# Performance work log

Hardware: AMD Instinct MI355X
Metric: run time of the kernel (lower is better)

The kernel has to match this reference:

```python
import jax, jax.numpy as jnp
import numpy as np

TAU = 2.0      # LIF membrane time constant
ALPHA = 4.0    # spikingjelly surrogate.Sigmoid default alpha
V_TH = 1.0     # LIF threshold
EPS = 1e-5     # BatchNorm eps
NUM_HEADS = 8
TOPK = 64      # int(0.25 * 256)


@jax.custom_vjp
def spike_fn(x):
    # Heaviside spike with sigmoid surrogate gradient
    return (x >= 0.0).astype(x.dtype)

def _spike_fwd(x):
    return spike_fn(x), x

def _spike_bwd(x, g):
    s = jax.nn.sigmoid(ALPHA * x)
    return (g * ALPHA * s * (1.0 - s),)

spike_fn.defvjp(_spike_fwd, _spike_bwd)


def lif(x_seq):
    # Multi-step LIF (decay_input=True, hard reset to 0, detach_reset=True).
    # x_seq: [T, ...]; returns spikes of same shape.
    def step(v, x):
        v = v + (x - v) / TAU
        s = spike_fn(v - V_TH)
        v = v * (1.0 - jax.lax.stop_gradient(s))
        return v, s
    _, spikes = jax.lax.scan(step, jnp.zeros_like(x_seq[0]), x_seq)
    return spikes


def bn_eval(x, p):
    # BatchNorm in eval mode over last axis; p rows = [gamma, beta, mean, var]
    gamma, beta, mean, var = p[0], p[1], p[2], p[3]
    return (x - mean) * (gamma * jax.lax.rsqrt(var + EPS)) + beta


def setup_inputs() -> dict:
    key = jax.random.key(0)
    ks = jax.random.split(key, 10)
    T, B, N, C, H = 4, 16, 256, 256, NUM_HEADS
    w_scale = C ** -0.5
    return {
        "x": jax.random.normal(ks[0], (T, B, N, C), jnp.float32),
        "wq": jax.random.normal(ks[1], (C, C), jnp.float32) * w_scale,
        "wk": jax.random.normal(ks[2], (C, C), jnp.float32) * w_scale,
        "wv": jax.random.normal(ks[3], (C, C), jnp.float32) * w_scale,
        "bnq": jax.random.uniform(ks[4], (4, C), jnp.float32, 0.1, 1.0),
        "bnk": jax.random.uniform(ks[5], (4, C), jnp.float32, 0.1, 1.0),
        "bnv": jax.random.uniform(ks[6], (4, C), jnp.float32, 0.1, 1.0),
        "proj_w": jax.random.normal(ks[7], (C, C), jnp.float32) * w_scale,
        "proj_bn": jax.random.uniform(ks[8], (4, C), jnp.float32, 0.1, 1.0),
        "rel_bias_table": jax.random.normal(ks[9], (2 * N - 1, H), jnp.float32),
    }


def reference(x, wq, wk, wv, bnq, bnk, bnv, proj_w, proj_bn, rel_bias_table):
    T, B, N, C = x.shape
    H = NUM_HEADS
    D = C // H
    scale = C ** -0.5

    def qkv_branch(w, bn_p):
        h = jnp.einsum('tbnc,oc->tbno', x, w)   # Linear (no bias)
        h = bn_eval(h, bn_p)                    # eval BN is per-channel affine
        s = lif(h)                              # [T,B,N,C] spikes
        return s.reshape(T, B, N, H, D).transpose(0, 1, 3, 2, 4)  # [T,B,H,N,D]

    q = qkv_branch(wq, bnq)
    k = qkv_branch(wk, bnk)
    v = qkv_branch(wv, bnv)

    attn = jnp.einsum('tbhnd,tbhmd->tbhnm', q, k) * scale  # [T,B,H,N,N]

    # relative position bias gather: table[(j - i) + (N-1)] -> [N,N,H]
    rel_idx = (jnp.arange(N)[None, :] - jnp.arange(N)[:, None]) + (N - 1)
    rel_bias = rel_bias_table[rel_idx]                      # [N,N,H]
    attn = attn + rel_bias.transpose(2, 0, 1)[None, None]   # bcast over T,B

    # top-k keep per row, others zeroed (no softmax)
    kth = jax.lax.stop_gradient(jax.lax.top_k(attn, TOPK)[0][..., -1:])
    attn = jnp.where(attn >= kth, attn, 0.0)

    out = jnp.einsum('tbhnm,tbhmd->tbhnd', attn, v)
    out = out.transpose(0, 1, 3, 2, 4).reshape(T, B, N, C)
    out = lif(out)  # attn_lif

    # proj SpikLinearLayer: Linear -> BN(eval) -> LIF
    h = jnp.einsum('tbnc,oc->tbno', out, proj_w)
    h = bn_eval(h, proj_bn)
    return lif(h)
```

## Files before the change

### kernel.cpp

```cpp
#include <hip/hip_runtime.h>

typedef unsigned int u32;
typedef unsigned long long u64;

#define T_ 4
#define B_ 16
#define N_ 256
#define C_ 256
#define H_ 8
#define D_ 32
#define BNC_ 1048576
#define NELEM 4194304

__global__ __launch_bounds__(128) void gemm_bn(
    const float* __restrict__ A, const float* __restrict__ W,
    const float* __restrict__ bnp, float* __restrict__ Out)
{
  __shared__ float As[32][132];
  __shared__ float Ws[32][68];
  const int tid = threadIdx.x;
  const int m0 = blockIdx.y << 7;
  const int n0 = blockIdx.x << 6;
  const int tx = tid & 7;
  const int ty = tid >> 3;

  float acc[8][8] = {};
  float4 pa[8], pb[4];

#define LOADA(k0)                                                          \
  _Pragma("unroll") for (int c = 0; c < 8; ++c) {                          \
    int id2 = tid + (c << 7); int row = id2 >> 3; int k4 = (id2 & 7) << 2; \
    pa[c] = *(const float4*)(A + (size_t)(m0 + row) * 256 + (k0) + k4);    \
  }
#define LOADB(k0)                                                          \
  _Pragma("unroll") for (int c = 0; c < 4; ++c) {                          \
    int id2 = tid + (c << 7); int row = id2 >> 3; int k4 = (id2 & 7) << 2; \
    pb[c] = *(const float4*)(W + (size_t)(n0 + row) * 256 + (k0) + k4);    \
  }

  LOADA(0); LOADB(0);

  for (int s = 0; s < 8; ++s) {
#pragma unroll
    for (int c = 0; c < 8; ++c) {
      int id2 = tid + (c << 7); int row = id2 >> 3; int k4 = (id2 & 7) << 2;
      As[k4+0][row] = pa[c].x; As[k4+1][row] = pa[c].y;
      As[k4+2][row] = pa[c].z; As[k4+3][row] = pa[c].w;
    }
#pragma unroll
    for (int c = 0; c < 4; ++c) {
      int id2 = tid + (c << 7); int row = id2 >> 3; int k4 = (id2 & 7) << 2;
      Ws[k4+0][row] = pb[c].x; Ws[k4+1][row] = pb[c].y;
      Ws[k4+2][row] = pb[c].z; Ws[k4+3][row] = pb[c].w;
    }
    __syncthreads();
    if (s < 7) { int k0n = (s + 1) << 5; LOADA(k0n); LOADB(k0n); }
#pragma unroll
    for (int kk = 0; kk < 32; ++kk) {
      float4 a0 = *(const float4*)&As[kk][ty << 3];
      float4 a1 = *(const float4*)&As[kk][(ty << 3) + 4];
      float4 b0 = *(const float4*)&Ws[kk][tx << 3];
      float4 b1 = *(const float4*)&Ws[kk][(tx << 3) + 4];
      float av[8] = {a0.x,a0.y,a0.z,a0.w,a1.x,a1.y,a1.z,a1.w};
      float bv[8] = {b0.x,b0.y,b0.z,b0.w,b1.x,b1.y,b1.z,b1.w};
#pragma unroll
      for (int ii = 0; ii < 8; ++ii)
#pragma unroll
        for (int jj = 0; jj < 8; ++jj)
          acc[ii][jj] = fmaf(av[ii], bv[jj], acc[ii][jj]);
    }
    __syncthreads();
  }

  const float* gma = bnp;
  const float* bta = bnp + 256;
  const float* mea = bnp + 512;
  const float* vra = bnp + 768;
  float sc[8], me[8], be[8];
#pragma unroll
  for (int jj = 0; jj < 8; ++jj) {
    int o = n0 + (tx << 3) + jj;
    sc[jj] = __fmul_rn(gma[o], 1.0f / sqrtf(__fadd_rn(vra[o], 1e-5f)));
    me[jj] = mea[o];
    be[jj] = bta[o];
  }
#pragma unroll
  for (int ii = 0; ii < 8; ++ii) {
    int row = m0 + (ty << 3) + ii;
    float4 y0, y1;
    y0.x = __fadd_rn(__fmul_rn(__fsub_rn(acc[ii][0], me[0]), sc[0]), be[0]);
    y0.y = __fadd_rn(__fmul_rn(__fsub_rn(acc[ii][1], me[1]), sc[1]), be[1]);
    y0.z = __fadd_rn(__fmul_rn(__fsub_rn(acc[ii][2], me[2]), sc[2]), be[2]);
    y0.w = __fadd_rn(__fmul_rn(__fsub_rn(acc[ii][3], me[3]), sc[3]), be[3]);
    y1.x = __fadd_rn(__fmul_rn(__fsub_rn(acc[ii][4], me[4]), sc[4]), be[4]);
    y1.y = __fadd_rn(__fmul_rn(__fsub_rn(acc[ii][5], me[5]), sc[5]), be[5]);
    y1.z = __fadd_rn(__fmul_rn(__fsub_rn(acc[ii][6], me[6]), sc[6]), be[6]);
    y1.w = __fadd_rn(__fmul_rn(__fsub_rn(acc[ii][7], me[7]), sc[7]), be[7]);
    *(float4*)(Out + (size_t)row * 256 + n0 + (tx << 3))     = y0;
    *(float4*)(Out + (size_t)row * 256 + n0 + (tx << 3) + 4) = y1;
  }
}

__global__ __launch_bounds__(256) void lif_pack3(
    const float* __restrict__ h0, const float* __restrict__ h1,
    const float* __restrict__ h2,
    u32* __restrict__ m0p, u32* __restrict__ m1p, u32* __restrict__ m2p)
{
  const float* h = (blockIdx.y == 0) ? h0 : (blockIdx.y == 1) ? h1 : h2;
  u32* mask      = (blockIdx.y == 0) ? m0p : (blockIdx.y == 1) ? m1p : m2p;
  const int blk = blockIdx.x;
  const int b = blk >> 8, n = blk & 255;
  const int c = threadIdx.x;
  const int wave = c >> 6, lane = c & 63;
  const size_t idx = ((size_t)b * 256 + n) * 256 + c;
  float v = 0.0f;
#pragma unroll
  for (int t = 0; t < 4; ++t) {
    float xv = h[idx + (size_t)t * BNC_];
    v = __fadd_rn(v, __fmul_rn(__fsub_rn(xv, v), 0.5f));
    bool s = (v >= 1.0f);
    u64 bal = __ballot(s);
    const int h0i = wave << 1;
    u32* mptr = mask + ((size_t)(t * 16 + b) * 8) * 256 + n;
    if (lane == 0)  mptr[(size_t)h0i * 256]       = (u32)bal;
    if (lane == 32) mptr[(size_t)(h0i + 1) * 256] = (u32)(bal >> 32);
    v = s ? 0.0f : v;
  }
}

__global__ __launch_bounds__(256) void attn_topk_pv(
    const u32* __restrict__ qmask, const u32* __restrict__ kmask,
    const u32* __restrict__ vmask, const float* __restrict__ table,
    float* __restrict__ outPV)
{
  __shared__ __align__(16) float bias[511];
  __shared__ __align__(16) u64 comp[4][2][132];

  const int tbh = blockIdx.x;
  const int rg = blockIdx.y;
  const int hh = tbh & 7;
  const int tid = threadIdx.x;

  bias[tid] = table[tid * 8 + hh];
  if (tid < 255) bias[256 + tid] = table[(256 + tid) * 8 + hh];
  __syncthreads();

  const int wave = tid >> 6, lane = tid & 63;
  const int d = lane & 31, half = lane >> 5;

  u32 kmr[4], vmr[4];
#pragma unroll
  for (int r = 0; r < 4; ++r) {
    kmr[r] = kmask[((size_t)tbh << 8) + lane + (r << 6)];
    vmr[r] = vmask[((size_t)tbh << 8) + lane + (r << 6)];
  }
  const u64 below = (1ull << lane) - 1ull;
  u64* const clo = &comp[wave][0][0];
  u64* const chi = &comp[wave][1][0];

#pragma unroll 1
  for (int it = 0; it < 8; ++it) {
    const int i = (rg << 5) + (it << 2) + wave;
    const u32 qm = qmask[((size_t)tbh << 8) + i];
    float a[4]; u32 u[4];
#pragma unroll
    for (int r = 0; r < 4; ++r) {
      const int j = lane + (r << 6);
      const int m = __popc(qm & kmr[r]);
      float av = __fmul_rn((float)m, 0.0625f);
      av = __fadd_rn(av, bias[j - i + 255]);
      a[r] = av;
      const u32 bb = __float_as_uint(av);
      u[r] = bb ^ ((u32)((int)bb >> 31) | 0x80000000u);
    }
    u32 t = 0u;
    for (int bit = 31; bit >= 0; --bit) {
      const u32 cand = t | (1u << bit);
      const int cnt = __popcll(__ballot(u[0] >= cand)) +
                      __popcll(__ballot(u[1] >= cand)) +
                      __popcll(__ballot(u[2] >= cand)) +
                      __popcll(__ballot(u[3] >= cand));
      if (cnt >= 64) { t = cand; if (cnt == 64) break; }
    }
    const u64 B0 = __ballot(u[0] >= t), B1 = __ballot(u[1] >= t);
    const u64 B2 = __ballot(u[2] >= t), B3 = __ballot(u[3] >= t);
    const int c0 = __popcll(B0), c1 = __popcll(B1);
    const int c2 = __popcll(B2), c3 = __popcll(B3);
    const int p0 = __popcll(B0 & below);
    const int p1 = c0 + __popcll(B1 & below);
    const int p2 = __popcll(B2 & below);
    const int p3 = c2 + __popcll(B3 & below);
    if (u[0] >= t) clo[p0] = ((u64)vmr[0] << 32) | (u64)__float_as_uint(a[0]);
    if (u[1] >= t) clo[p1] = ((u64)vmr[1] << 32) | (u64)__float_as_uint(a[1]);
    if (u[2] >= t) chi[p2] = ((u64)vmr[2] << 32) | (u64)__float_as_uint(a[2]);
    if (u[3] >= t) chi[p3] = ((u64)vmr[3] << 32) | (u64)__float_as_uint(a[3]);
    const int nlo = c0 + c1, nhi = c2 + c3;
    if (lane < 2)      clo[nlo + lane] = 0ull;
    else if (lane < 4) chi[nhi + lane - 2] = 0ull;
    asm volatile("s_waitcnt lgkmcnt(0)" ::: "memory");

    const int n = half ? nhi : nlo;
    const u64* cp = half ? chi : clo;
    const int gn = (n + 1) >> 1;
    float s = 0.0f;
    for (int g = 0; g < gn; ++g) {
      uint4 e = *(const uint4*)(cp + ((size_t)g << 1));
      const u32 mk0 = (u32)__builtin_amdgcn_sbfe((int)e.y, d, 1);
      s = __fadd_rn(s, __uint_as_float(e.x & mk0));
      const u32 mk1 = (u32)__builtin_amdgcn_sbfe((int)e.w, d, 1);
      s = __fadd_rn(s, __uint_as_float(e.z & mk1));
    }
    s += __shfl_xor(s, 32, 64);
    if (half == 0)
      outPV[(((size_t)tbh << 8) + i) * 32 + d] = s;
  }
}

__global__ __launch_bounds__(256) void attn_lif(
    const float* __restrict__ pv, float* __restrict__ sout)
{
  const int blk = blockIdx.x;
  const int b = blk >> 8, n = blk & 255;
  const int c = threadIdx.x;
  const int hh = c >> 5, d = c & 31;
  float v = 0.0f;
#pragma unroll
  for (int t = 0; t < 4; ++t) {
    float xv = pv[(((size_t)(t * 16 + b) * 8 + hh) << 13) + (n << 5) + d];
    v = __fadd_rn(v, __fmul_rn(__fsub_rn(xv, v), 0.5f));
    bool s = (v >= 1.0f);
    sout[(((size_t)(t * 16 + b) << 8) + n) * 256 + c] = s ? 1.0f : 0.0f;
    v = s ? 0.0f : v;
  }
}

__global__ __launch_bounds__(256) void final_lif(
    const float* __restrict__ hp, float* __restrict__ out)
{
  const size_t base = (size_t)blockIdx.x * 256 + threadIdx.x;
  float v = 0.0f;
#pragma unroll
  for (int t = 0; t < 4; ++t) {
    float xv = hp[base + (size_t)t * BNC_];
    v = __fadd_rn(v, __fmul_rn(__fsub_rn(xv, v), 0.5f));
    bool s = (v >= 1.0f);
    out[base + (size_t)t * BNC_] = s ? 1.0f : 0.0f;
    v = s ? 0.0f : v;
  }
}

extern "C" void kernel_launch(void* const* d_in, const int* in_sizes, int n_in,
                              void* d_out, int out_size, void* d_ws, size_t ws_size,
                              hipStream_t stream) {
  const float* x       = (const float*)d_in[0];
  const float* wq      = (const float*)d_in[1];
  const float* wk      = (const float*)d_in[2];
  const float* wv      = (const float*)d_in[3];
  const float* bnq     = (const float*)d_in[4];
  const float* bnk     = (const float*)d_in[5];
  const float* bnv     = (const float*)d_in[6];
  const float* proj_w  = (const float*)d_in[7];
  const float* proj_bn = (const float*)d_in[8];
  const float* rtable  = (const float*)d_in[9];
  float* out = (float*)d_out;

  float* ws = (float*)d_ws;
  float* hq = ws;
  float* hk = ws + (size_t)NELEM;
  float* hv = ws + (size_t)NELEM * 2;
  u32* mq = (u32*)(ws + (size_t)NELEM * 3);
  u32* mk = mq + 131072;
  u32* mv = mk + 131072;
  float* outPV = hq;
  float* sout  = hk;
  float* hproj = hv;

  dim3 ggrid(4, 128);
  gemm_bn<<<ggrid, 128, 0, stream>>>(x, wq, bnq, hq);
  gemm_bn<<<ggrid, 128, 0, stream>>>(x, wk, bnk, hk);
  gemm_bn<<<ggrid, 128, 0, stream>>>(x, wv, bnv, hv);

  lif_pack3<<<dim3(4096, 3), 256, 0, stream>>>(hq, hk, hv, mq, mk, mv);

  attn_topk_pv<<<dim3(512, 8), 256, 0, stream>>>(mq, mk, mv, rtable, outPV);

  attn_lif<<<4096, 256, 0, stream>>>(outPV, sout);

  gemm_bn<<<ggrid, 128, 0, stream>>>(sout, proj_w, proj_bn, hproj);

  final_lif<<<4096, 256, 0, stream>>>(hproj, out);
}
```

Before: 335.3 us.

## Fuse QKV GEMMs into one kernel sharing A tile, with pre-transposed weights

Replaces the per-weight shared-memory tiled GEMM with a templated kernel that stages one 256-row A tile in LDS and reads the weights directly from global memory as a pre-transposed layout. Q, K and V are computed in a single launch that reuses the same A tile across all three weights. A new transpose kernel rewrites all four weight matrices each call. This cuts three launches and three reads of x down to one, but the weight operand now comes from cache/global instead of LDS with a 4xCW register tile per lane. Double-buffered prefetch is also dropped.

```diff
diff --git a/kernel.cpp b/kernel.cpp
--- a/kernel.cpp
+++ b/kernel.cpp
@@ -12,92 +12,110 @@
 #define BNC_ 1048576
 #define NELEM 4194304
 
-__global__ __launch_bounds__(128) void gemm_bn(
-    const float* __restrict__ A, const float* __restrict__ W,
-    const float* __restrict__ bnp, float* __restrict__ Out)
-{
-  __shared__ float As[32][132];
-  __shared__ float Ws[32][68];
+__global__ __launch_bounds__(256) void transpose4(
+    const float* __restrict__ w0, const float* __restrict__ w1,
+    const float* __restrict__ w2, const float* __restrict__ w3,
+    float* __restrict__ wt)
+{
+  __shared__ float t[32][33];
+  const float* src = (blockIdx.z == 0) ? w0 : (blockIdx.z == 1) ? w1
+                   : (blockIdx.z == 2) ? w2 : w3;
+  float* dst = wt + ((size_t)blockIdx.z << 16);
+  const int lx = threadIdx.x & 31, ly = threadIdx.x >> 5;
+  const int x = (blockIdx.x << 5) + lx;
+  const int y0 = (blockIdx.y << 5) + ly;
+#pragma unroll
+  for (int r = 0; r < 32; r += 8)
+    t[ly + r][lx] = src[(size_t)(y0 + r) * 256 + x];
+  __syncthreads();
+  const int xo = (blockIdx.y << 5) + lx;
+  const int yo = (blockIdx.x << 5) + ly;
+#pragma unroll
+  for (int r = 0; r < 32; r += 8)
+    dst[(size_t)(yo + r) * 256 + xo] = t[lx][ly + r];
+}
+
+template<int NW, int CW>
+__global__ __launch_bounds__(256) void gemm_bn_t(
+    const float* __restrict__ A, const float* __restrict__ WTb,
+    const float* __restrict__ bn0, const float* __restrict__ bn1,
+    const float* __restrict__ bn2,
+    float* __restrict__ O0, float* __restrict__ O1, float* __restrict__ O2)
+{
+  __shared__ float As[32][260];
   const int tid = threadIdx.x;
-  const int m0 = blockIdx.y << 7;
-  const int n0 = blockIdx.x << 6;
-  const int tx = tid & 7;
-  const int ty = tid >> 3;
-
-  float acc[8][8] = {};
-  float4 pa[8], pb[4];
-
-#define LOADA(k0)                                                          \
-  _Pragma("unroll") for (int c = 0; c < 8; ++c) {                          \
-    int id2 = tid + (c << 7); int row = id2 >> 3; int k4 = (id2 & 7) << 2; \
-    pa[c] = *(const float4*)(A + (size_t)(m0 + row) * 256 + (k0) + k4);    \
-  }
-#define LOADB(k0)                                                          \
-  _Pragma("unroll") for (int c = 0; c < 4; ++c) {                          \
-    int id2 = tid + (c << 7); int row = id2 >> 3; int k4 = (id2 & 7) << 2; \
-    pb[c] = *(const float4*)(W + (size_t)(n0 + row) * 256 + (k0) + k4);    \
-  }
-
-  LOADA(0); LOADB(0);
+  const int wave = tid >> 6, lane = tid & 63;
+  const int m0 = blockIdx.y << 8;
+  const int col0 = blockIdx.x * (4 * CW) + wave * CW;
+  const int sr = tid >> 3;
+  const int sk = (tid & 7) << 2;
+  const int row4 = lane << 2;
+
+  const float* bnp[3] = {bn0, bn1, bn2};
+  float* Op[3] = {O0, O1, O2};
+
+  float acc[NW][4][CW] = {};
 
   for (int s = 0; s < 8; ++s) {
+    const int k0 = s << 5;
+    float4 pa[8];
+#pragma unroll
+    for (int c = 0; c < 8; ++c)
+      pa[c] = *(const float4*)(A + (size_t)(m0 + sr + (c << 5)) * 256 + k0 + sk);
+    __syncthreads();
 #pragma unroll
     for (int c = 0; c < 8; ++c) {
-      int id2 = tid + (c << 7); int row = id2 >> 3; int k4 = (id2 & 7) << 2;
-      As[k4+0][row] = pa[c].x; As[k4+1][row] = pa[c].y;
-      As[k4+2][row] = pa[c].z; As[k4+3][row] = pa[c].w;
-    }
-#pragma unroll
-    for (int c = 0; c < 4; ++c) {
-      int id2 = tid + (c << 7); int row = id2 >> 3; int k4 = (id2 & 7) << 2;
-      Ws[k4+0][row] = pb[c].x; Ws[k4+1][row] = pb[c].y;
-      Ws[k4+2][row] = pb[c].z; Ws[k4+3][row] = pb[c].w;
+      As[sk + 0][sr + (c << 5)] = pa[c].x;
+      As[sk + 1][sr + (c << 5)] = pa[c].y;
+      As[sk + 2][sr + (c << 5)] = pa[c].z;
+      As[sk + 3][sr + (c << 5)] = pa[c].w;
     }
     __syncthreads();
-    if (s < 7) { int k0n = (s + 1) << 5; LOADA(k0n); LOADB(k0n); }
-#pragma unroll
+#pragma unroll 4
     for (int kk = 0; kk < 32; ++kk) {
-      float4 a0 = *(const float4*)&As[kk][ty << 3];
-      float4 a1 = *(const float4*)&As[kk][(ty << 3) + 4];
-      float4 b0 = *(const float4*)&Ws[kk][tx << 3];
-      float4 b1 = *(const float4*)&Ws[kk][(tx << 3) + 4];
-      float av[8] = {a0.x,a0.y,a0.z,a0.w,a1.x,a1.y,a1.z,a1.w};
-      float bv[8] = {b0.x,b0.y,b0.z,b0.w,b1.x,b1.y,b1.z,b1.w};
-#pragma unroll
-      for (int ii = 0; ii < 8; ++ii)
-#pragma unroll
-        for (int jj = 0; jj < 8; ++jj)
-          acc[ii][jj] = fmaf(av[ii], bv[jj], acc[ii][jj]);
-    }
-    __syncthreads();
-  }
-
-  const float* gma = bnp;
-  const float* bta = bnp + 256;
-  const float* mea = bnp + 512;
-  const float* vra = bnp + 768;
-  float sc[8], me[8], be[8];
-#pragma unroll
-  for (int jj = 0; jj < 8; ++jj) {
-    int o = n0 + (tx << 3) + jj;
-    sc[jj] = __fmul_rn(gma[o], 1.0f / sqrtf(__fadd_rn(vra[o], 1e-5f)));
-    me[jj] = mea[o];
-    be[jj] = bta[o];
-  }
-#pragma unroll
-  for (int ii = 0; ii < 8; ++ii) {
-    int row = m0 + (ty << 3) + ii;
-    float4 y0, y1;
-    y0.x = __fadd_rn(__fmul_rn(__fsub_rn(acc[ii][0], me[0]), sc[0]), be[0]);
-    y0.y = __fadd_rn(__fmul_rn(__fsub_rn(acc[ii][1], me[1]), sc[1]), be[1]);
-    y0.z = __fadd_rn(__fmul_rn(__fsub_rn(acc[ii][2], me[2]), sc[2]), be[2]);
-    y0.w = __fadd_rn(__fmul_rn(__fsub_rn(acc[ii][3], me[3]), sc[3]), be[3]);
-    y1.x = __fadd_rn(__fmul_rn(__fsub_rn(acc[ii][4], me[4]), sc[4]), be[4]);
-    y1.y = __fadd_rn(__fmul_rn(__fsub_rn(acc[ii][5], me[5]), sc[5]), be[5]);
-    y1.z = __fadd_rn(__fmul_rn(__fsub_rn(acc[ii][6], me[6]), sc[6]), be[6]);
-    y1.w = __fadd_rn(__fmul_rn(__fsub_rn(acc[ii][7], me[7]), sc[7]), be[7]);
-    *(float4*)(Out + (size_t)row * 256 + n0 + (tx << 3))     = y0;
-    *(float4*)(Out + (size_t)row * 256 + n0 + (tx << 3) + 4) = y1;
+      const float4 av = *(const float4*)&As[kk][row4];
+      const float ar[4] = {av.x, av.y, av.z, av.w};
+#pragma unroll
+      for (int w = 0; w < NW; ++w) {
+#pragma unroll
+        for (int cq = 0; cq < CW / 4; ++cq) {
+          const float4 b4 = *(const float4*)(
+              WTb + ((size_t)w << 16) + (size_t)(k0 + kk) * 256 + col0 + (cq << 2));
+          const float br[4] = {b4.x, b4.y, b4.z, b4.w};
+#pragma unroll
+          for (int r = 0; r < 4; ++r)
+#pragma unroll
+            for (int j = 0; j < 4; ++j)
+              acc[w][r][(cq << 2) + j] =
+                  fmaf(ar[r], br[j], acc[w][r][(cq << 2) + j]);
+        }
+      }
+    }
+  }
+
+#pragma unroll
+  for (int w = 0; w < NW; ++w) {
+    float sc[CW], me[CW], be[CW];
+#pragma unroll
+    for (int j = 0; j < CW; ++j) {
+      const int o = col0 + j;
+      sc[j] = __fmul_rn(bnp[w][o], 1.0f / sqrtf(__fadd_rn(bnp[w][768 + o], 1e-5f)));
+      me[j] = bnp[w][512 + o];
+      be[j] = bnp[w][256 + o];
+    }
+#pragma unroll
+    for (int r = 0; r < 4; ++r) {
+      float* outp = Op[w] + (size_t)(m0 + row4 + r) * 256 + col0;
+#pragma unroll
+      for (int cq = 0; cq < CW / 4; ++cq) {
+        float4 y;
+        y.x = __fadd_rn(__fmul_rn(__fsub_rn(acc[w][r][cq*4+0], me[cq*4+0]), sc[cq*4+0]), be[cq*4+0]);
+        y.y = __fadd_rn(__fmul_rn(__fsub_rn(acc[w][r][cq*4+1], me[cq*4+1]), sc[cq*4+1]), be[cq*4+1]);
+        y.z = __fadd_rn(__fmul_rn(__fsub_rn(acc[w][r][cq*4+2], me[cq*4+2]), sc[cq*4+2]), be[cq*4+2]);
+        y.w = __fadd_rn(__fmul_rn(__fsub_rn(acc[w][r][cq*4+3], me[cq*4+3]), sc[cq*4+3]), be[cq*4+3]);
+        *(float4*)(outp + (cq << 2)) = y;
+      }
+    }
   }
 }
 
@@ -271,14 +289,15 @@
   u32* mq = (u32*)(ws + (size_t)NELEM * 3);
   u32* mk = mq + 131072;
   u32* mv = mk + 131072;
+  float* wt = (float*)(mv + 131072);
   float* outPV = hq;
   float* sout  = hk;
   float* hproj = hv;
 
-  dim3 ggrid(4, 128);
-  gemm_bn<<<ggrid, 128, 0, stream>>>(x, wq, bnq, hq);
-  gemm_bn<<<ggrid, 128, 0, stream>>>(x, wk, bnk, hk);
-  gemm_bn<<<ggrid, 128, 0, stream>>>(x, wv, bnv, hv);
+  transpose4<<<dim3(8, 8, 4), 256, 0, stream>>>(wq, wk, wv, proj_w, wt);
+
+  gemm_bn_t<3, 4><<<dim3(16, 64), 256, 0, stream>>>(
+      x, wt, bnq, bnk, bnv, hq, hk, hv);
 
   lif_pack3<<<dim3(4096, 3), 256, 0, stream>>>(hq, hk, hv, mq, mk, mv);
 
@@ -286,7 +305,8 @@
 
   attn_lif<<<4096, 256, 0, stream>>>(outPV, sout);
 
-  gemm_bn<<<ggrid, 128, 0, stream>>>(sout, proj_w, proj_bn, hproj);
+  gemm_bn_t<1, 8><<<dim3(8, 64), 256, 0, stream>>>(
+      sout, wt + 3 * 65536, proj_bn, proj_bn, proj_bn, hproj, hproj, hproj);
 
   final_lif<<<4096, 256, 0, stream>>>(hproj, out);
 }
```

New measurement: 437.0 us. 30.3% more time.
